# Performance work log

Hardware: AMD Instinct MI355X
Metric: run time of the kernel (lower is better)

## Reference

```python
import jax, jax.numpy as jnp
import numpy as np

SCALING = 2.0      # lora_alpha / r = 32 / 16
TEMPERATURE = 1.0  # router_temperature


def setup_inputs() -> dict:
    key = jax.random.key(0)
    ks = jax.random.split(key, 7)
    B, S, D, K, R = 4, 2048, 4096, 8, 16
    # Note: torch inits lora_B to zeros; we use small random values so the
    return {
        "x": jax.random.normal(ks[0], (B, S, D), dtype=jnp.float32),
        "base_w": jax.random.normal(ks[1], (D, D), dtype=jnp.float32) * 0.02,
        "base_b": jax.random.normal(ks[2], (D,), dtype=jnp.float32) * 0.02,
        "lora_A": jax.random.normal(ks[3], (K, R, D), dtype=jnp.float32) * 0.02,
        "lora_B": jax.random.normal(ks[4], (K, D, R), dtype=jnp.float32) * 0.02,
        "router_w": jax.random.normal(ks[5], (K, D), dtype=jnp.float32) * 0.02,
        "router_b": jnp.zeros((K,), dtype=jnp.float32),
    }


def reference(x, base_w, base_b, lora_A, lora_B, router_w, router_b):
    # base_layer(x): x @ W^T + b
    base = jnp.einsum("bsd,od->bso", x, base_w) + base_b
    # router on mean-pooled sequence (x.dim()==3 branch): softmax(Linear(mean_s x))
    router_in = x.mean(axis=1)                                   # [B, D]
    logits = router_in @ router_w.T + router_b                   # [B, K]
    weights = jax.nn.softmax(logits / TEMPERATURE, axis=-1)      # [B, K]
    # grouped LoRA experts: h = A_k x, out = sum_k w_k * B_k h  (dropout p=0 -> identity)
    h = jnp.einsum("bsd,krd->bskr", x, lora_A)                   # [B, S, K, R]
    lora = jnp.einsum("bskr,kor,bk->bso", h, lora_B, weights)    # [B, S, D]
    return base + SCALING * lora
```

## Files before the change

### kernel.cpp

```cpp
#include <hip/hip_runtime.h>
#include <hip/hip_fp16.h>
#include <stdint.h>

typedef _Float16 f16;
typedef __attribute__((ext_vector_type(8))) _Float16 f16x8;
typedef __attribute__((ext_vector_type(4))) float f32x4;

#define D_DIM 4096
#define S_DIM 2048
#define M_DIM 8192
#define R_DIM 16
#define KR 128
#define KTOT 4224
#define NKT 66
#define SCALING 2.0f

#define WS_AP    0
#define WS_WP    69206016
#define WS_AH    103809024
#define WS_HP    104857600
#define WS_PART  121634816
#define WS_LG    123731968
#define WS_WS    123732096

__device__ __forceinline__ void load_lds16(const void* g, void* l) {
  __builtin_amdgcn_global_load_lds(
      (const __attribute__((address_space(1))) void*)g,
      (__attribute__((address_space(3))) void*)l, 16, 0, 0);
}

union H4 { f16 h[4]; ushort4 u; };

__global__ void conv_x(const float* __restrict__ x, f16* __restrict__ Ap,
                       float* __restrict__ part) {
  int rc = blockIdx.x;
  int cc = blockIdx.y;
  int col = cc * 1024 + threadIdx.x * 4;
  long base = (long)rc * 64 * D_DIM + col;
  float s0 = 0, s1 = 0, s2 = 0, s3 = 0;
  for (int r = 0; r < 64; ++r) {
    float4 v = *(const float4*)(x + base + (long)r * D_DIM);
    H4 t; t.h[0] = (f16)v.x; t.h[1] = (f16)v.y; t.h[2] = (f16)v.z; t.h[3] = (f16)v.w;
    *(ushort4*)((char*)Ap + ((long)(rc * 64 + r) * KTOT + col) * 2) = t.u;
    s0 += v.x; s1 += v.y; s2 += v.z; s3 += v.w;
  }
  float4 sv; sv.x = s0; sv.y = s1; sv.z = s2; sv.w = s3;
  *(float4*)(part + (long)rc * D_DIM + col) = sv;
}

__global__ void conv_w(const float* __restrict__ w, f16* __restrict__ Wp) {
  int rc = blockIdx.x;
  int cc = blockIdx.y;
  int col = cc * 1024 + threadIdx.x * 4;
  long base = (long)rc * 64 * D_DIM + col;
  for (int r = 0; r < 64; ++r) {
    float4 v = *(const float4*)(w + base + (long)r * D_DIM);
    H4 t; t.h[0] = (f16)v.x; t.h[1] = (f16)v.y; t.h[2] = (f16)v.z; t.h[3] = (f16)v.w;
    *(ushort4*)((char*)Wp + ((long)(rc * 64 + r) * KTOT + col) * 2) = t.u;
  }
}

__global__ void conv_bext(const float* __restrict__ loraB, f16* __restrict__ Wp) {
  int g = blockIdx.x * 256 + threadIdx.x;
  int n = g >> 7, kr = g & 127;
  int k = kr >> 4, r = kr & 15;
  float v = loraB[((long)k * D_DIM + n) * R_DIM + r];
  Wp[(long)n * KTOT + D_DIM + kr] = (f16)v;
}

__global__ void conv_aext(const float* __restrict__ loraA, f16* __restrict__ Ah) {
  long g = ((long)blockIdx.x * 256 + threadIdx.x) * 4;
  float4 v = *(const float4*)(loraA + g);
  H4 t; t.h[0] = (f16)v.x; t.h[1] = (f16)v.y; t.h[2] = (f16)v.z; t.h[3] = (f16)v.w;
  *(ushort4*)((char*)Ah + g * 2) = t.u;
}

__global__ void router_logits(const float* __restrict__ part, const float* __restrict__ rw,
                              const float* __restrict__ rb, float* __restrict__ logits) {
  int b = blockIdx.x >> 3, k = blockIdx.x & 7;
  const float* w = rw + k * D_DIM;
  float p = 0.f;
  for (int d = threadIdx.x; d < D_DIM; d += 256) {
    float s = 0.f;
    #pragma unroll 8
    for (int i = 0; i < 32; ++i) s += part[(long)(b * 32 + i) * D_DIM + d];
    p += s * w[d];
  }
  __shared__ float red[4];
  for (int off = 32; off; off >>= 1) p += __shfl_down(p, off);
  if ((threadIdx.x & 63) == 0) red[threadIdx.x >> 6] = p;
  __syncthreads();
  if (threadIdx.x == 0)
    logits[b * 8 + k] = (red[0] + red[1] + red[2] + red[3]) / (float)S_DIM + rb[k];
}

__global__ void router_softmax(const float* __restrict__ logits, float* __restrict__ wsc) {
  int lane = threadIdx.x;
  if (lane < 32) {
    float L = logits[lane];
    float m = L;
    m = fmaxf(m, __shfl_xor(m, 1));
    m = fmaxf(m, __shfl_xor(m, 2));
    m = fmaxf(m, __shfl_xor(m, 4));
    float e = __expf(L - m);
    float s = e;
    s += __shfl_xor(s, 1); s += __shfl_xor(s, 2); s += __shfl_xor(s, 4);
    wsc[lane] = e / s * SCALING;
  }
}

__global__ void combine_h(const float* __restrict__ hp, const float* __restrict__ wsc,
                          f16* __restrict__ Ap) {
  long g = (long)blockIdx.x * 256 + threadIdx.x;
  long row = g >> 7; int kr = (int)(g & 127);
  int b = (int)(row >> 11);
  float s = hp[g] + hp[g + 1048576] + hp[g + 2097152] + hp[g + 3145728];
  Ap[row * KTOT + D_DIM + kr] = (f16)(s * wsc[b * 8 + (kr >> 4)]);
}

__device__ __forceinline__ void stage256(const f16* __restrict__ G, long row0, int ld,
                                         long kbase, char* ldsT, int tid) {
  int lr = tid >> 3;
  int sw = (((tid & 7) * 16) ^ ((lr & 7) << 4)) >> 1;
  char* wbase = ldsT + ((tid >> 6) << 10);
  #pragma unroll
  for (int j = 0; j < 4; ++j) {
    const f16* g = G + (row0 + j * 64 + lr) * (long)ld + kbase + sw;
    load_lds16(g, wbase + j * 8192);
  }
}
__device__ __forceinline__ void stage128(const f16* __restrict__ G, long row0, int ld,
                                         long kbase, char* ldsT, int tid) {
  int lr = tid >> 3;
  int sw = (((tid & 7) * 16) ^ ((lr & 7) << 4)) >> 1;
  char* wbase = ldsT + ((tid >> 6) << 10);
  #pragma unroll
  for (int j = 0; j < 4; ++j) {
    const f16* g = G + (row0 + j * 32 + lr) * (long)ld + kbase + sw;
    load_lds16(g, wbase + j * 4096);
  }
}

__global__ __launch_bounds__(256, 2) void gemm_h2(
    const f16* __restrict__ A, int lda, const f16* __restrict__ Bt, int ldb,
    float* __restrict__ hp) {
  __shared__ __align__(16) char smem[65536];
  int tid = threadIdx.x;
  int wave = tid >> 6, lane = tid & 63;
  int wr = wave >> 1, wc = wave & 1;
  int fr = lane & 15, fq = lane >> 4;
  long row0 = (long)blockIdx.x * 128;
  long koff = (long)blockIdx.y * 1024;

  f32x4 acc[4][4] = {};

  stage128(A,  row0, lda, koff,      smem,         tid);
  stage128(Bt, 0,    ldb, koff,      smem + 16384, tid);
  stage128(A,  row0, lda, koff + 64, smem + 32768, tid);
  stage128(Bt, 0,    ldb, koff + 64, smem + 49152, tid);
  asm volatile("s_waitcnt vmcnt(8)" ::: "memory");
  asm volatile("s_barrier" ::: "memory");

  int cur = 0;
  int sw = (fr & 7) << 4;
  for (int t = 0; t < 16; ++t) {
    const char* Ab = smem + cur * 32768;
    const char* Bb = Ab + 16384;
    __builtin_amdgcn_s_setprio(1);
    #pragma unroll
    for (int ks = 0; ks < 2; ++ks) {
      int kb = ks * 64 + fq * 16;
      f16x8 af[4], bf[4];
      #pragma unroll
      for (int mi = 0; mi < 4; ++mi)
        af[mi] = *(const f16x8*)(Ab + (wr * 64 + mi * 16 + fr) * 128 + (kb ^ sw));
      #pragma unroll
      for (int ni = 0; ni < 4; ++ni)
        bf[ni] = *(const f16x8*)(Bb + (wc * 64 + ni * 16 + fr) * 128 + (kb ^ sw));
      #pragma unroll
      for (int mi = 0; mi < 4; ++mi)
        #pragma unroll
        for (int ni = 0; ni < 4; ++ni)
          acc[mi][ni] = __builtin_amdgcn_mfma_f32_16x16x32_f16(af[mi], bf[ni], acc[mi][ni], 0, 0, 0);
    }
    __builtin_amdgcn_s_setprio(0);
    asm volatile("s_barrier" ::: "memory");
    if (t + 2 < 16) {
      stage128(A,  row0, lda, koff + (t + 2) * 64, smem + cur * 32768,         tid);
      stage128(Bt, 0,    ldb, koff + (t + 2) * 64, smem + cur * 32768 + 16384, tid);
      asm volatile("s_waitcnt vmcnt(8)" ::: "memory");
    } else {
      asm volatile("s_waitcnt vmcnt(0)" ::: "memory");
    }
    asm volatile("s_barrier" ::: "memory");
    cur ^= 1;
  }

  long zb = (long)blockIdx.y * (long)M_DIM * 128;
  #pragma unroll
  for (int ni = 0; ni < 4; ++ni) {
    int col = wc * 64 + ni * 16 + fr;
    #pragma unroll
    for (int mi = 0; mi < 4; ++mi) {
      long row = row0 + wr * 64 + mi * 16 + fq * 4;
      float* cp = hp + zb + row * 128 + col;
      #pragma unroll
      for (int j = 0; j < 4; ++j) cp[(long)j * 128] = acc[mi][ni][j];
    }
  }
}

__global__ __launch_bounds__(512, 2) void gemm256(
    const f16* __restrict__ A, int lda, const f16* __restrict__ Bt, int ldb,
    int nkt, const float* __restrict__ bias, float* __restrict__ C, int ldc) {
  __shared__ __align__(16) char smem[131072];
  int tid = threadIdx.x;
  int wave = tid >> 6, lane = tid & 63;
  int wr = wave >> 2, wc = wave & 3;
  int fr = lane & 15, fq = lane >> 4;

  int flat = blockIdx.x;
  int wg = (flat & 7) * 64 + (flat >> 3);
  long row0 = (long)(wg >> 4) * 256;
  long col0 = (long)(wg & 15) * 256;

  f32x4 acc[8][4] = {};

  stage256(A,  row0, lda, 0,  smem,          tid);
  stage256(Bt, col0, ldb, 0,  smem + 32768,  tid);
  stage256(A,  row0, lda, 64, smem + 65536,  tid);
  stage256(Bt, col0, ldb, 64, smem + 98304,  tid);
  asm volatile("s_waitcnt vmcnt(8)" ::: "memory");
  asm volatile("s_barrier" ::: "memory");

  int cur = 0;
  int sw = (fr & 7) << 4;
  for (int t = 0; t < nkt; ++t) {
    const char* Ab = smem + cur * 65536;
    const char* Bb = Ab + 32768;
    __builtin_amdgcn_s_setprio(1);
    #pragma unroll
    for (int qm = 0; qm < 2; ++qm) {
      f16x8 af[4][2];
      #pragma unroll
      for (int m2 = 0; m2 < 4; ++m2) {
        int row = wr * 128 + (qm * 4 + m2) * 16 + fr;
        af[m2][0] = *(const f16x8*)(Ab + row * 128 + ((fq * 16) ^ sw));
        af[m2][1] = *(const f16x8*)(Ab + row * 128 + ((64 + fq * 16) ^ sw));
      }
      #pragma unroll
      for (int qn = 0; qn < 2; ++qn) {
        f16x8 bf[2][2];
        #pragma unroll
        for (int n2 = 0; n2 < 2; ++n2) {
          int rowb = wc * 64 + (qn * 2 + n2) * 16 + fr;
          bf[n2][0] = *(const f16x8*)(Bb + rowb * 128 + ((fq * 16) ^ sw));
          bf[n2][1] = *(const f16x8*)(Bb + rowb * 128 + ((64 + fq * 16) ^ sw));
        }
        #pragma unroll
        for (int m2 = 0; m2 < 4; ++m2)
          #pragma unroll
          for (int n2 = 0; n2 < 2; ++n2) {
            f32x4* a = &acc[qm * 4 + m2][qn * 2 + n2];
            *a = __builtin_amdgcn_mfma_f32_16x16x32_f16(af[m2][0], bf[n2][0], *a, 0, 0, 0);
            *a = __builtin_amdgcn_mfma_f32_16x16x32_f16(af[m2][1], bf[n2][1], *a, 0, 0, 0);
          }
      }
    }
    __builtin_amdgcn_s_setprio(0);
    asm volatile("s_barrier" ::: "memory");
    if (t + 2 < nkt) {
      stage256(A,  row0, lda, (long)(t + 2) * 64, smem + cur * 65536,         tid);
      stage256(Bt, col0, ldb, (long)(t + 2) * 64, smem + cur * 65536 + 32768, tid);
      asm volatile("s_waitcnt vmcnt(8)" ::: "memory");
    } else {
      asm volatile("s_waitcnt vmcnt(0)" ::: "memory");
    }
    asm volatile("s_barrier" ::: "memory");
    cur ^= 1;
  }

  #pragma unroll
  for (int ni = 0; ni < 4; ++ni) {
    long col = col0 + wc * 64 + ni * 16 + fr;
    float bv = bias[col];
    #pragma unroll
    for (int mi = 0; mi < 8; ++mi) {
      long row = row0 + wr * 128 + mi * 16 + fq * 4;
      float* cp = C + row * ldc + col;
      #pragma unroll
      for (int j = 0; j < 4; ++j) cp[(long)j * ldc] = acc[mi][ni][j] + bv;
    }
  }
}

extern "C" void kernel_launch(void* const* d_in, const int* in_sizes, int n_in,
                              void* d_out, int out_size, void* d_ws, size_t ws_size,
                              hipStream_t stream) {
  (void)in_sizes; (void)n_in; (void)out_size; (void)ws_size;
  const float* x        = (const float*)d_in[0];
  const float* base_w   = (const float*)d_in[1];
  const float* base_b   = (const float*)d_in[2];
  const float* lora_A   = (const float*)d_in[3];
  const float* lora_B   = (const float*)d_in[4];
  const float* router_w = (const float*)d_in[5];
  const float* router_b = (const float*)d_in[6];
  float* out = (float*)d_out;

  char* ws = (char*)d_ws;
  f16* Ap       = (f16*)(ws + WS_AP);
  f16* Wp       = (f16*)(ws + WS_WP);
  f16* Ah       = (f16*)(ws + WS_AH);
  float* hp     = (float*)(ws + WS_HP);
  float* part   = (float*)(ws + WS_PART);
  float* logits = (float*)(ws + WS_LG);
  float* wsc    = (float*)(ws + WS_WS);

  conv_x<<<dim3(128, 4), 256, 0, stream>>>(x, Ap, part);
  conv_w<<<dim3(64, 4), 256, 0, stream>>>(base_w, Wp);
  conv_bext<<<2048, 256, 0, stream>>>(lora_B, Wp);
  conv_aext<<<512, 256, 0, stream>>>(lora_A, Ah);
  router_logits<<<32, 256, 0, stream>>>(part, router_w, router_b, logits);
  router_softmax<<<1, 64, 0, stream>>>(logits, wsc);
  gemm_h2<<<dim3(64, 4), 256, 0, stream>>>(Ap, KTOT, Ah, D_DIM, hp);
  combine_h<<<4096, 256, 0, stream>>>(hp, wsc, Ap);
  gemm256<<<512, 512, 0, stream>>>(Ap, KTOT, Wp, KTOT, NKT, base_b, out, D_DIM);
}
```

Before: 588.7 us.

## Switch main GEMM to 32-wide K tiles with a 4-stage LDS ring

The main 256x256 GEMM now stages K in 32-element slices into a four-buffer LDS ring, prefetching three tiles ahead instead of two 64-wide double buffers. It also uses a new swizzle for 64-byte rows and issues one barrier pair per 32-K step. The setprio hints are removed from both GEMMs. The intent is deeper prefetch to hide global latency, at the cost of twice as many iterations and barriers with less MFMA work between them.

```diff
diff --git a/kernel.cpp b/kernel.cpp
--- a/kernel.cpp
+++ b/kernel.cpp
@@ -12,7 +12,7 @@
 #define R_DIM 16
 #define KR 128
 #define KTOT 4224
-#define NKT 66
+#define NKT32 132
 #define SCALING 2.0f
 
 #define WS_AP    0
@@ -118,17 +118,6 @@
   Ap[row * KTOT + D_DIM + kr] = (f16)(s * wsc[b * 8 + (kr >> 4)]);
 }
 
-__device__ __forceinline__ void stage256(const f16* __restrict__ G, long row0, int ld,
-                                         long kbase, char* ldsT, int tid) {
-  int lr = tid >> 3;
-  int sw = (((tid & 7) * 16) ^ ((lr & 7) << 4)) >> 1;
-  char* wbase = ldsT + ((tid >> 6) << 10);
-  #pragma unroll
-  for (int j = 0; j < 4; ++j) {
-    const f16* g = G + (row0 + j * 64 + lr) * (long)ld + kbase + sw;
-    load_lds16(g, wbase + j * 8192);
-  }
-}
 __device__ __forceinline__ void stage128(const f16* __restrict__ G, long row0, int ld,
                                          long kbase, char* ldsT, int tid) {
   int lr = tid >> 3;
@@ -138,6 +127,18 @@
   for (int j = 0; j < 4; ++j) {
     const f16* g = G + (row0 + j * 32 + lr) * (long)ld + kbase + sw;
     load_lds16(g, wbase + j * 4096);
+  }
+}
+__device__ __forceinline__ void stage32(const f16* __restrict__ G, long row0, int ld,
+                                        long kbase, char* ldsT, int tid) {
+  int r = tid >> 2;
+  int c = (tid & 3) * 16;
+  int swc = (c ^ (((r >> 1) & 3) << 4)) >> 1;
+  char* wbase = ldsT + ((tid >> 6) << 10);
+  #pragma unroll
+  for (int j = 0; j < 2; ++j) {
+    const f16* g = G + (row0 + j * 128 + r) * (long)ld + kbase + swc;
+    load_lds16(g, wbase + j * 8192);
   }
 }
 
@@ -166,7 +167,6 @@
   for (int t = 0; t < 16; ++t) {
     const char* Ab = smem + cur * 32768;
     const char* Bb = Ab + 16384;
-    __builtin_amdgcn_s_setprio(1);
     #pragma unroll
     for (int ks = 0; ks < 2; ++ks) {
       int kb = ks * 64 + fq * 16;
@@ -183,7 +183,6 @@
         for (int ni = 0; ni < 4; ++ni)
           acc[mi][ni] = __builtin_amdgcn_mfma_f32_16x16x32_f16(af[mi], bf[ni], acc[mi][ni], 0, 0, 0);
     }
-    __builtin_amdgcn_s_setprio(0);
     asm volatile("s_barrier" ::: "memory");
     if (t + 2 < 16) {
       stage128(A,  row0, lda, koff + (t + 2) * 64, smem + cur * 32768,         tid);
@@ -226,58 +225,45 @@
 
   f32x4 acc[8][4] = {};
 
-  stage256(A,  row0, lda, 0,  smem,          tid);
-  stage256(Bt, col0, ldb, 0,  smem + 32768,  tid);
-  stage256(A,  row0, lda, 64, smem + 65536,  tid);
-  stage256(Bt, col0, ldb, 64, smem + 98304,  tid);
+  stage32(A,  row0, lda, 0,  smem,                 tid);
+  stage32(Bt, col0, ldb, 0,  smem + 16384,         tid);
+  stage32(A,  row0, lda, 32, smem + 32768,         tid);
+  stage32(Bt, col0, ldb, 32, smem + 32768 + 16384, tid);
+  stage32(A,  row0, lda, 64, smem + 65536,         tid);
+  stage32(Bt, col0, ldb, 64, smem + 65536 + 16384, tid);
   asm volatile("s_waitcnt vmcnt(8)" ::: "memory");
   asm volatile("s_barrier" ::: "memory");
 
-  int cur = 0;
-  int sw = (fr & 7) << 4;
+  int sw = (fq * 16) ^ (((fr >> 1) & 3) << 4);
   for (int t = 0; t < nkt; ++t) {
-    const char* Ab = smem + cur * 65536;
-    const char* Bb = Ab + 32768;
-    __builtin_amdgcn_s_setprio(1);
-    #pragma unroll
-    for (int qm = 0; qm < 2; ++qm) {
-      f16x8 af[4][2];
-      #pragma unroll
-      for (int m2 = 0; m2 < 4; ++m2) {
-        int row = wr * 128 + (qm * 4 + m2) * 16 + fr;
-        af[m2][0] = *(const f16x8*)(Ab + row * 128 + ((fq * 16) ^ sw));
-        af[m2][1] = *(const f16x8*)(Ab + row * 128 + ((64 + fq * 16) ^ sw));
-      }
-      #pragma unroll
-      for (int qn = 0; qn < 2; ++qn) {
-        f16x8 bf[2][2];
-        #pragma unroll
-        for (int n2 = 0; n2 < 2; ++n2) {
-          int rowb = wc * 64 + (qn * 2 + n2) * 16 + fr;
-          bf[n2][0] = *(const f16x8*)(Bb + rowb * 128 + ((fq * 16) ^ sw));
-          bf[n2][1] = *(const f16x8*)(Bb + rowb * 128 + ((64 + fq * 16) ^ sw));
-        }
-        #pragma unroll
-        for (int m2 = 0; m2 < 4; ++m2)
-          #pragma unroll
-          for (int n2 = 0; n2 < 2; ++n2) {
-            f32x4* a = &acc[qm * 4 + m2][qn * 2 + n2];
-            *a = __builtin_amdgcn_mfma_f32_16x16x32_f16(af[m2][0], bf[n2][0], *a, 0, 0, 0);
-            *a = __builtin_amdgcn_mfma_f32_16x16x32_f16(af[m2][1], bf[n2][1], *a, 0, 0, 0);
-          }
-      }
-    }
-    __builtin_amdgcn_s_setprio(0);
+    const char* Ab = smem + (t & 3) * 32768;
+    const char* Bb = Ab + 16384;
+    f16x8 af[8], bf[4];
+    #pragma unroll
+    for (int m2 = 0; m2 < 8; ++m2)
+      af[m2] = *(const f16x8*)(Ab + (wr * 128 + m2 * 16 + fr) * 64 + sw);
+    #pragma unroll
+    for (int n2 = 0; n2 < 4; ++n2)
+      bf[n2] = *(const f16x8*)(Bb + (wc * 64 + n2 * 16 + fr) * 64 + sw);
+    #pragma unroll
+    for (int m2 = 0; m2 < 8; ++m2)
+      #pragma unroll
+      for (int n2 = 0; n2 < 4; ++n2)
+        acc[m2][n2] = __builtin_amdgcn_mfma_f32_16x16x32_f16(af[m2], bf[n2], acc[m2][n2], 0, 0, 0);
+
+    if (t + 1 >= nkt) break;
     asm volatile("s_barrier" ::: "memory");
-    if (t + 2 < nkt) {
-      stage256(A,  row0, lda, (long)(t + 2) * 64, smem + cur * 65536,         tid);
-      stage256(Bt, col0, ldb, (long)(t + 2) * 64, smem + cur * 65536 + 32768, tid);
-      asm volatile("s_waitcnt vmcnt(8)" ::: "memory");
-    } else {
-      asm volatile("s_waitcnt vmcnt(0)" ::: "memory");
-    }
+    if (t + 3 < nkt) {
+      char* dst = smem + ((t + 3) & 3) * 32768;
+      stage32(A,  row0, lda, (long)(t + 3) * 32, dst,         tid);
+      stage32(Bt, col0, ldb, (long)(t + 3) * 32, dst + 16384, tid);
+    }
+    int hi = (t + 3 < nkt) ? (t + 3) : (nkt - 1);
+    int cnt = (hi - (t + 1)) * 4;
+    if (cnt == 8)      asm volatile("s_waitcnt vmcnt(8)" ::: "memory");
+    else if (cnt == 4) asm volatile("s_waitcnt vmcnt(4)" ::: "memory");
+    else               asm volatile("s_waitcnt vmcnt(0)" ::: "memory");
     asm volatile("s_barrier" ::: "memory");
-    cur ^= 1;
   }
 
   #pragma unroll
@@ -324,5 +310,5 @@
   router_softmax<<<1, 64, 0, stream>>>(logits, wsc);
   gemm_h2<<<dim3(64, 4), 256, 0, stream>>>(Ap, KTOT, Ah, D_DIM, hp);
   combine_h<<<4096, 256, 0, stream>>>(hp, wsc, Ap);
-  gemm256<<<512, 512, 0, stream>>>(Ap, KTOT, Wp, KTOT, NKT, base_b, out, D_DIM);
-}
+  gemm256<<<512, 512, 0, stream>>>(Ap, KTOT, Wp, KTOT, NKT32, base_b, out, D_DIM);
+}
```

Result: slower. 627.5 us (+6.6%).
